# Optimization experiments

Measured on AMD Instinct MI355X. Metric: run time of the kernel, lower is better.

The kernel has to match this reference:

```python
import jax, jax.numpy as jnp
import numpy as np

EMB = 128
B, N = 8, 4096

def setup_inputs() -> dict:
    key = jax.random.key(0)
    k_x, k_q, k_k, k_v = jax.random.split(key, 4)
    return {
        "x": jax.random.normal(k_x, (B, N, EMB), dtype=jnp.float32),
        "w_query": jax.random.uniform(k_q, (EMB, EMB), dtype=jnp.float32),
        "w_key": jax.random.uniform(k_k, (EMB, EMB), dtype=jnp.float32),
        "w_value": jax.random.uniform(k_v, (EMB, EMB), dtype=jnp.float32),
    }

def reference(x, w_query, w_key, w_value):
    # QKV projections: [B, N, D]
    q = jnp.einsum("bnd,de->bne", x, w_query)
    k = jnp.einsum("bnd,de->bne", x, w_key)
    v = jnp.einsum("bnd,de->bne", x, w_value)
    dk = k.shape[-1]
    # scaled dot-product scores: [B, N, N]
    scale = jnp.einsum("bqd,bkd->bqk", q, k) / jnp.sqrt(jnp.float32(dk))
    probs = jax.nn.softmax(scale, axis=2)
    # attention output: [B, N, D]
    return jnp.einsum("bqk,bkd->bqd", probs, v)
```

## Files before the change

kernel.cpp:

```cpp
#include <hip/hip_runtime.h>
#include <hip/hip_bf16.h>

typedef __attribute__((ext_vector_type(4))) float  f32x4;
typedef __attribute__((ext_vector_type(8))) _Float16 h16x8;
typedef __attribute__((ext_vector_type(2))) __fp16 fp16x2;
typedef const __attribute__((address_space(1))) unsigned int guint;
typedef __attribute__((address_space(3))) unsigned int luint;

#define EMB 128
#define NSEQ 4096
#define NB 8
#define SCALE 0.08838834764831845f
#define QSC   (0.08838834764831845f * 1.44269504f)
#define NT    (NSEQ / 64)

#if __has_builtin(__builtin_amdgcn_exp2f)
#define EXP2(x) __builtin_amdgcn_exp2f(x)
#else
#define EXP2(x) exp2f(x)
#endif

__global__ void prep_w(const float* __restrict__ wq, const float* __restrict__ wk,
                       const float* __restrict__ wv, _Float16* __restrict__ whiT,
                       _Float16* __restrict__ wloT) {
    int idx = blockIdx.x * 256 + threadIdx.x;
    if (idx >= 3 * EMB * EMB) return;
    int widx = idx >> 14;
    int rem  = idx & 16383;
    int d = rem >> 7;
    int e = rem & 127;
    const float* w = (widx == 0) ? wq : (widx == 1) ? wk : wv;
    float v = w[d * 128 + e];
    _Float16 hi = (_Float16)v;
    _Float16 lo = (_Float16)(v - (float)hi);
    whiT[(size_t)widx * 16384 + (size_t)e * 128 + d] = hi;
    wloT[(size_t)widx * 16384 + (size_t)e * 128 + d] = lo;
}

__global__ __launch_bounds__(256) void qkv_proj(const float* __restrict__ x,
                                                const _Float16* __restrict__ whiT,
                                                const _Float16* __restrict__ wloT,
                                                _Float16* __restrict__ q,
                                                char* __restrict__ kimg,
                                                char* __restrict__ vimg,
                                                float* __restrict__ aq,
                                                float* __restrict__ ck) {
    const int widx = blockIdx.x >> 9;
    const int blk  = blockIdx.x & 511;
    const int lane = threadIdx.x & 63;
    const int wave = threadIdx.x >> 6;
    const int g    = lane >> 4;
    const int lr   = lane & 15;
    const int rb   = blk * 64 + wave * 16;

    h16x8 xhi[4], xlo[4];
    {
        const float* xrow = x + (size_t)(rb + lr) * EMB;
        #pragma unroll
        for (int kc = 0; kc < 4; ++kc) {
            const float* p = xrow + kc * 32 + g * 8;
            h16x8 ah, al;
            #pragma unroll
            for (int j = 0; j < 8; ++j) {
                float v = p[j];
                _Float16 h = (_Float16)v;
                ah[j] = h;
                al[j] = (_Float16)(v - (float)h);
            }
            xhi[kc] = ah;
            if (widx < 2) xlo[kc] = al;
        }
    }

    const int b  = rb >> 12;
    const int n0 = rb & 4095;

    f32x4 acc[8];
    #pragma unroll
    for (int ct = 0; ct < 8; ++ct) acc[ct] = (f32x4){0.f, 0.f, 0.f, 0.f};

    const _Float16* wh = whiT + (size_t)widx * 16384;
    const _Float16* wl = wloT + (size_t)widx * 16384;
    #pragma unroll
    for (int kc = 0; kc < 4; ++kc) {
        #pragma unroll
        for (int ct = 0; ct < 8; ++ct) {
            size_t off = (size_t)(ct * 16 + lr) * 128 + kc * 32 + g * 8;
            h16x8 bh = *(const h16x8*)(wh + off);
            acc[ct] = __builtin_amdgcn_mfma_f32_16x16x32_f16(xhi[kc], bh, acc[ct], 0, 0, 0);
            if (widx < 2) {
                h16x8 bl = *(const h16x8*)(wl + off);
                acc[ct] = __builtin_amdgcn_mfma_f32_16x16x32_f16(xlo[kc], bh, acc[ct], 0, 0, 0);
                acc[ct] = __builtin_amdgcn_mfma_f32_16x16x32_f16(xhi[kc], bl, acc[ct], 0, 0, 0);
            }
        }
    }

    if (widx < 2) {
        float c[4];
        #pragma unroll
        for (int r = 0; r < 4; ++r) {
            float rs = 0.f;
            #pragma unroll
            for (int ct = 0; ct < 8; ++ct) rs += acc[ct][r];
            #pragma unroll
            for (int off = 8; off; off >>= 1) rs += __shfl_xor(rs, off);
            c[r] = rs * (1.0f / 128.0f);
        }
        if (widx == 0) {
            #pragma unroll
            for (int ct = 0; ct < 8; ++ct)
                #pragma unroll
                for (int r = 0; r < 4; ++r) {
                    size_t row = rb + g * 4 + r;
                    q[row * 128 + ct * 16 + lr] = (_Float16)((acc[ct][r] - c[r]) * QSC);
                }
            if (lr == 0) {
                #pragma unroll
                for (int r = 0; r < 4; ++r) aq[rb + g * 4 + r] = c[r] * 128.0f * QSC;
            }
        } else {
            #pragma unroll
            for (int ct = 0; ct < 8; ++ct)
                #pragma unroll
                for (int r = 0; r < 4; ++r) {
                    int nn  = n0 + g * 4 + r;
                    int tt  = nn >> 6, r64 = nn & 63;
                    int slot = ((r64 >> 5) * 2 + ((r64 >> 2) & 1)) * 16
                             + (((r64 >> 3) & 3) << 2) + (r64 & 3);
                    int e = ct * 16 + lr;
                    size_t byte = ((size_t)(b * 64 + tt) << 14) + slot * 256
                                + ((2 * e) ^ ((slot & 15) << 4));
                    *(_Float16*)(kimg + byte) = (_Float16)(acc[ct][r] - c[r]);
                }
            if (lr == 0) {
                #pragma unroll
                for (int r = 0; r < 4; ++r) ck[rb + g * 4 + r] = c[r];
            }
        }
    } else {
        #pragma unroll
        for (int ct = 0; ct < 8; ++ct)
            #pragma unroll
            for (int r = 0; r < 4; ++r) {
                int e  = ct * 16 + lr;
                int nn = n0 + g * 4 + r;
                int tt = nn >> 6, kv = nn & 63;
                size_t byte = ((size_t)(b * 64 + tt) << 14) + e * 128
                            + ((2 * kv) ^ ((e & 7) << 4));
                *(_Float16*)(vimg + byte) = (_Float16)acc[ct][r];
            }
    }
}

__global__ __launch_bounds__(256, 2) void flash(const _Float16* __restrict__ q,
                                                const char* __restrict__ kimg,
                                                const char* __restrict__ vimg,
                                                const float* __restrict__ aq,
                                                const float* __restrict__ ck,
                                                float* __restrict__ O0,
                                                float* __restrict__ O1,
                                                float* __restrict__ m0a, float* __restrict__ l0a,
                                                float* __restrict__ m1a, float* __restrict__ l1a) {
    __shared__ __align__(16) char KsB[2][16384];
    __shared__ __align__(16) char VsB[2][16384];

    const int bp  = blockIdx.x;
    const int bid = (bp & 7) * 64 + (bp >> 3);

    const int lane = threadIdx.x & 63;
    const int wave = threadIdx.x >> 6;
    const int g    = lane >> 4;
    const int lr   = lane & 15;
    const int b    = bid >> 6;
    const int rem  = bid & 63;
    const int qt   = rem & 31;
    const int half = rem >> 5;
    const int t0   = half * (NT / 2);
    const size_t baseA = (size_t)b * NSEQ + qt * 128 + wave * 32;
    const size_t baseB = baseA + 16;

    float* __restrict__ Opart = half ? O1 : O0;
    float* __restrict__ mArr  = half ? m1a : m0a;
    float* __restrict__ lArr  = half ? l1a : l0a;

    const char* kimg_b = kimg + ((size_t)b << 20);
    const char* vimg_b = vimg + ((size_t)b << 20);
    const float* ckb   = ck + (size_t)b * NSEQ;

    h16x8 qfA[4], qfB[4];
    #pragma unroll
    for (int kc = 0; kc < 4; ++kc) {
        qfA[kc] = *(const h16x8*)(q + (baseA + lr) * 128 + kc * 32 + g * 8);
        qfB[kc] = *(const h16x8*)(q + (baseB + lr) * 128 + kc * 32 + g * 8);
    }
    const float aqvA = aq[baseA + lr];
    const float aqvB = aq[baseB + lr];

    auto stage = [&](int tile, int buf) {
        const char* ks = kimg_b + ((size_t)tile << 14) + wave * 4096 + lane * 16;
        const char* vs = vimg_b + ((size_t)tile << 14) + wave * 4096 + lane * 16;
        char* kd = (char*)KsB[buf] + wave * 4096;
        char* vd = (char*)VsB[buf] + wave * 4096;
        #pragma unroll
        for (int i = 0; i < 4; ++i) {
            __builtin_amdgcn_global_load_lds((guint*)(ks + i * 1024), (luint*)(kd + i * 1024), 16, 0, 0);
            __builtin_amdgcn_global_load_lds((guint*)(vs + i * 1024), (luint*)(vd + i * 1024), 16, 0, 0);
        }
    };

    stage(t0, 0);
    __syncthreads();

    f32x4 oA[8], oB[8];
    #pragma unroll
    for (int ct = 0; ct < 8; ++ct) {
        oA[ct] = (f32x4){0.f, 0.f, 0.f, 0.f};
        oB[ct] = (f32x4){0.f, 0.f, 0.f, 0.f};
    }
    float mA = -1e30f, mB = -1e30f;
    float lA = 0.f, lB = 0.f;

    int cur = 0;
    for (int t = t0; t < t0 + NT / 2; ++t) {
        int tn = (t + 1 < t0 + NT / 2) ? t + 1 : t;
        stage(tn, cur ^ 1);

        f32x4 ckt[4];
        #pragma unroll
        for (int ct = 0; ct < 4; ++ct)
            ckt[ct] = *(const f32x4*)(ckb + t * 64 + (ct >> 1) * 32 + (ct & 1) * 4 + g * 8);

        const char* Kb = KsB[cur];
        f32x4 sA[4], sB[4];
        __builtin_amdgcn_s_setprio(1);
        #pragma unroll
        for (int ct = 0; ct < 4; ++ct) {
            f32x4 aA = (f32x4){0.f, 0.f, 0.f, 0.f};
            f32x4 aB = (f32x4){0.f, 0.f, 0.f, 0.f};
            #pragma unroll
            for (int kc = 0; kc < 4; ++kc) {
                h16x8 kb = *(const h16x8*)(Kb + (ct * 16 + lr) * 256 + ((kc * 64 + g * 16) ^ (lr << 4)));
                aA = __builtin_amdgcn_mfma_f32_16x16x32_f16(kb, qfA[kc], aA, 0, 0, 0);
                aB = __builtin_amdgcn_mfma_f32_16x16x32_f16(kb, qfB[kc], aB, 0, 0, 0);
            }
            #pragma unroll
            for (int r = 0; r < 4; ++r) {
                aA[r] += aqvA * ckt[ct][r];
                aB[r] += aqvB * ckt[ct][r];
            }
            sA[ct] = aA;
            sB[ct] = aB;
        }
        __builtin_amdgcn_s_setprio(0);

        float tmA = sA[0][0], tmB = sB[0][0];
        #pragma unroll
        for (int ct = 0; ct < 4; ++ct)
            #pragma unroll
            for (int r = 0; r < 4; ++r) {
                tmA = fmaxf(tmA, sA[ct][r]);
                tmB = fmaxf(tmB, sB[ct][r]);
            }
        tmA = fmaxf(tmA, __shfl_xor(tmA, 16));
        tmA = fmaxf(tmA, __shfl_xor(tmA, 32));
        tmB = fmaxf(tmB, __shfl_xor(tmB, 16));
        tmB = fmaxf(tmB, __shfl_xor(tmB, 32));
        if (__any((tmA > mA + 11.544f) || (tmB > mB + 11.544f))) {
            float mnA = fmaxf(mA, tmA), mnB = fmaxf(mB, tmB);
            float scA = EXP2(mA - mnA), scB = EXP2(mB - mnB);
            mA = mnA; mB = mnB;
            lA *= scA; lB *= scB;
            float osA[4], osB[4];
            #pragma unroll
            for (int r = 0; r < 4; ++r) {
                osA[r] = __shfl(scA, (lane & 48) | (g * 4 + r));
                osB[r] = __shfl(scB, (lane & 48) | (g * 4 + r));
            }
            #pragma unroll
            for (int ct = 0; ct < 8; ++ct)
                #pragma unroll
                for (int r = 0; r < 4; ++r) {
                    oA[ct][r] *= osA[r];
                    oB[ct][r] *= osB[r];
                }
        }
        #pragma unroll
        for (int ct = 0; ct < 4; ++ct)
            #pragma unroll
            for (int r = 0; r < 4; ++r) {
                float pA = EXP2(sA[ct][r] - mA);
                float pB = EXP2(sB[ct][r] - mB);
                sA[ct][r] = pA; sB[ct][r] = pB;
                lA += pA; lB += pB;
            }

        union Pk { fp16x2 h2[4]; h16x8 v8; };
        h16x8 paA[2], paB[2];
        #pragma unroll
        for (int w = 0; w < 2; ++w) {
            Pk a, bk;
            a.h2[0]  = __builtin_amdgcn_cvt_pkrtz(sA[2 * w][0], sA[2 * w][1]);
            a.h2[1]  = __builtin_amdgcn_cvt_pkrtz(sA[2 * w][2], sA[2 * w][3]);
            a.h2[2]  = __builtin_amdgcn_cvt_pkrtz(sA[2 * w + 1][0], sA[2 * w + 1][1]);
            a.h2[3]  = __builtin_amdgcn_cvt_pkrtz(sA[2 * w + 1][2], sA[2 * w + 1][3]);
            bk.h2[0] = __builtin_amdgcn_cvt_pkrtz(sB[2 * w][0], sB[2 * w][1]);
            bk.h2[1] = __builtin_amdgcn_cvt_pkrtz(sB[2 * w][2], sB[2 * w][3]);
            bk.h2[2] = __builtin_amdgcn_cvt_pkrtz(sB[2 * w + 1][0], sB[2 * w + 1][1]);
            bk.h2[3] = __builtin_amdgcn_cvt_pkrtz(sB[2 * w + 1][2], sB[2 * w + 1][3]);
            paA[w] = a.v8;
            paB[w] = bk.v8;
        }

        const char* Vb = VsB[cur];
        __builtin_amdgcn_s_setprio(1);
        #pragma unroll
        for (int ct = 0; ct < 8; ++ct) {
            #pragma unroll
            for (int w = 0; w < 2; ++w) {
                h16x8 vb = *(const h16x8*)(Vb + (ct * 16 + lr) * 128 + ((w * 64 + g * 16) ^ ((lr & 7) << 4)));
                oA[ct] = __builtin_amdgcn_mfma_f32_16x16x32_f16(paA[w], vb, oA[ct], 0, 0, 0);
                oB[ct] = __builtin_amdgcn_mfma_f32_16x16x32_f16(paB[w], vb, oB[ct], 0, 0, 0);
            }
        }
        __builtin_amdgcn_s_setprio(0);

        __syncthreads();
        cur ^= 1;
    }

    lA += __shfl_xor(lA, 16);
    lA += __shfl_xor(lA, 32);
    lB += __shfl_xor(lB, 16);
    lB += __shfl_xor(lB, 32);
    if (lane < 16) {
        mArr[baseA + lr] = mA;  lArr[baseA + lr] = lA;
        mArr[baseB + lr] = mB;  lArr[baseB + lr] = lB;
    }
    #pragma unroll
    for (int ct = 0; ct < 8; ++ct)
        #pragma unroll
        for (int r = 0; r < 4; ++r) {
            size_t rowA = baseA + g * 4 + r;
            size_t rowB = baseB + g * 4 + r;
            Opart[rowA * EMB + ct * 16 + lr] = oA[ct][r];
            Opart[rowB * EMB + ct * 16 + lr] = oB[ct][r];
        }
}

__global__ __launch_bounds__(256) void merge_halves(const float* __restrict__ O1,
                                                    const float* __restrict__ m0a,
                                                    const float* __restrict__ l0a,
                                                    const float* __restrict__ m1a,
                                                    const float* __restrict__ l1a,
                                                    float* __restrict__ out) {
    int gid = blockIdx.x * 256 + threadIdx.x;
    int row = gid >> 4;
    int c0  = (gid & 15) * 8;
    float mm0 = m0a[row], mm1 = m1a[row];
    float M   = fmaxf(mm0, mm1);
    float w0  = EXP2(mm0 - M), w1 = EXP2(mm1 - M);
    float inv = 1.0f / (l0a[row] * w0 + l1a[row] * w1);
    float*       p0 = out + (size_t)row * EMB + c0;
    const float* p1 = O1  + (size_t)row * EMB + c0;
    f32x4 a0 = *(const f32x4*)p0, a1 = *(const f32x4*)(p0 + 4);
    f32x4 b0 = *(const f32x4*)p1, b1 = *(const f32x4*)(p1 + 4);
    f32x4 r0 = (a0 * w0 + b0 * w1) * inv;
    f32x4 r1 = (a1 * w0 + b1 * w1) * inv;
    *(f32x4*)p0       = r0;
    *(f32x4*)(p0 + 4) = r1;
}

extern "C" void kernel_launch(void* const* d_in, const int* in_sizes, int n_in,
                              void* d_out, int out_size, void* d_ws, size_t ws_size,
                              hipStream_t stream) {
    const float* x  = (const float*)d_in[0];
    const float* wq = (const float*)d_in[1];
    const float* wk = (const float*)d_in[2];
    const float* wv = (const float*)d_in[3];

    char* ws = (char*)d_ws;
    _Float16* q    = (_Float16*)(ws);
    char*     kimg = (char*)    (ws + 8388608);
    char*     vimg = (char*)    (ws + 16777216);
    float*    aq   = (float*)   (ws + 25165824);
    float*    ck   = (float*)   (ws + 25296896);
    _Float16* whiT = (_Float16*)(ws + 25427968);
    _Float16* wloT = (_Float16*)(ws + 25526272);
    float*    O1   = (float*)   (ws + 25690112);
    float*    m0a  = (float*)   (ws + 42467328);
    float*    l0a  = (float*)   (ws + 42598400);
    float*    m1a  = (float*)   (ws + 42729472);
    float*    l1a  = (float*)   (ws + 42860544);

    prep_w<<<192, 256, 0, stream>>>(wq, wk, wv, whiT, wloT);
    qkv_proj<<<1536, 256, 0, stream>>>(x, whiT, wloT, q, kimg, vimg, aq, ck);
    flash<<<512, 256, 0, stream>>>(q, kimg, vimg, aq, ck,
                                   (float*)d_out, O1, m0a, l0a, m1a, l1a);
    merge_halves<<<2048, 256, 0, stream>>>(O1, m0a, l0a, m1a, l1a, (float*)d_out);
}
```

Measured before the change: 143.7 us.

## Shrink KV tiles to 32, raise occupancy, and split KV four ways

Cuts the K/V tile from 64 to 32 keys, rewriting the K and V image layouts and swizzles so shared memory per block halves, and raises launch bounds to 4 blocks per SM. When the workspace is large enough, the key range is split into 4 chunks instead of 2, launching more blocks, and a generalized n-way merge kernel combines the partials. This aims to raise occupancy and parallelism so latency is better hidden. In exchange it adds more partial-output traffic, a heavier merge, and more loop iterations with synchronization per tile.

New measurement: 310.7 us. +116.3%, slower.

```diff
diff --git a/kernel.cpp b/kernel.cpp
--- a/kernel.cpp
+++ b/kernel.cpp
@@ -12,7 +12,7 @@
 #define NB 8
 #define SCALE 0.08838834764831845f
 #define QSC   (0.08838834764831845f * 1.44269504f)
-#define NT    (NSEQ / 64)
+#define NTT   (NSEQ / 32)
 
 #if __has_builtin(__builtin_amdgcn_exp2f)
 #define EXP2(x) __builtin_amdgcn_exp2f(x)
@@ -124,12 +124,11 @@
             for (int ct = 0; ct < 8; ++ct)
                 #pragma unroll
                 for (int r = 0; r < 4; ++r) {
-                    int nn  = n0 + g * 4 + r;
-                    int tt  = nn >> 6, r64 = nn & 63;
-                    int slot = ((r64 >> 5) * 2 + ((r64 >> 2) & 1)) * 16
-                             + (((r64 >> 3) & 3) << 2) + (r64 & 3);
-                    int e = ct * 16 + lr;
-                    size_t byte = ((size_t)(b * 64 + tt) << 14) + slot * 256
+                    int nn   = n0 + g * 4 + r;
+                    int tt   = nn >> 5, r32 = nn & 31;
+                    int slot = ((r32 >> 2) & 1) * 16 + (r32 >> 3) * 4 + (r32 & 3);
+                    int e    = ct * 16 + lr;
+                    size_t byte = ((size_t)(b * 128 + tt) << 13) + slot * 256
                                 + ((2 * e) ^ ((slot & 15) << 4));
                     *(_Float16*)(kimg + byte) = (_Float16)(acc[ct][r] - c[r]);
                 }
@@ -145,44 +144,46 @@
             for (int r = 0; r < 4; ++r) {
                 int e  = ct * 16 + lr;
                 int nn = n0 + g * 4 + r;
-                int tt = nn >> 6, kv = nn & 63;
-                size_t byte = ((size_t)(b * 64 + tt) << 14) + e * 128
-                            + ((2 * kv) ^ ((e & 7) << 4));
+                int tt = nn >> 5, kv = nn & 31;
+                size_t byte = ((size_t)(b * 128 + tt) << 13) + e * 64
+                            + ((2 * kv) ^ (((e >> 1) & 3) << 4));
                 *(_Float16*)(vimg + byte) = (_Float16)acc[ct][r];
             }
     }
 }
 
-__global__ __launch_bounds__(256, 2) void flash(const _Float16* __restrict__ q,
+__global__ __launch_bounds__(256, 4) void flash(const _Float16* __restrict__ q,
                                                 const char* __restrict__ kimg,
                                                 const char* __restrict__ vimg,
                                                 const float* __restrict__ aq,
                                                 const float* __restrict__ ck,
                                                 float* __restrict__ O0,
-                                                float* __restrict__ O1,
-                                                float* __restrict__ m0a, float* __restrict__ l0a,
-                                                float* __restrict__ m1a, float* __restrict__ l1a) {
-    __shared__ __align__(16) char KsB[2][16384];
-    __shared__ __align__(16) char VsB[2][16384];
-
-    const int bp  = blockIdx.x;
-    const int bid = (bp & 7) * 64 + (bp >> 3);
+                                                float* __restrict__ Oext,
+                                                float* __restrict__ mArr,
+                                                float* __restrict__ lArr,
+                                                int nsplit, int cnt) {
+    __shared__ __align__(16) char KsB[2][8192];
+    __shared__ __align__(16) char VsB[2][8192];
+
+    const int nblk = 256 * nsplit;
+    const int bp   = blockIdx.x;
+    const int bid  = (bp & 7) * (nblk >> 3) + (bp >> 3);
 
     const int lane = threadIdx.x & 63;
     const int wave = threadIdx.x >> 6;
     const int g    = lane >> 4;
     const int lr   = lane & 15;
-    const int b    = bid >> 6;
-    const int rem  = bid & 63;
-    const int qt   = rem & 31;
-    const int half = rem >> 5;
-    const int t0   = half * (NT / 2);
+    const int sp   = bid % nsplit;
+    const int rest = bid / nsplit;
+    const int qt   = rest & 31;
+    const int b    = rest >> 5;
+    const int t0   = sp * cnt;
     const size_t baseA = (size_t)b * NSEQ + qt * 128 + wave * 32;
     const size_t baseB = baseA + 16;
 
-    float* __restrict__ Opart = half ? O1 : O0;
-    float* __restrict__ mArr  = half ? m1a : m0a;
-    float* __restrict__ lArr  = half ? l1a : l0a;
+    float* __restrict__ Opart = (sp == 0) ? O0 : Oext + (size_t)(sp - 1) * NB * NSEQ * EMB;
+    float* __restrict__ mOut  = mArr + (size_t)sp * (NB * NSEQ);
+    float* __restrict__ lOut  = lArr + (size_t)sp * (NB * NSEQ);
 
     const char* kimg_b = kimg + ((size_t)b << 20);
     const char* vimg_b = vimg + ((size_t)b << 20);
@@ -198,12 +199,12 @@
     const float aqvB = aq[baseB + lr];
 
     auto stage = [&](int tile, int buf) {
-        const char* ks = kimg_b + ((size_t)tile << 14) + wave * 4096 + lane * 16;
-        const char* vs = vimg_b + ((size_t)tile << 14) + wave * 4096 + lane * 16;
-        char* kd = (char*)KsB[buf] + wave * 4096;
-        char* vd = (char*)VsB[buf] + wave * 4096;
-        #pragma unroll
-        for (int i = 0; i < 4; ++i) {
+        const char* ks = kimg_b + ((size_t)tile << 13) + wave * 2048 + lane * 16;
+        const char* vs = vimg_b + ((size_t)tile << 13) + wave * 2048 + lane * 16;
+        char* kd = (char*)KsB[buf] + wave * 2048;
+        char* vd = (char*)VsB[buf] + wave * 2048;
+        #pragma unroll
+        for (int i = 0; i < 2; ++i) {
             __builtin_amdgcn_global_load_lds((guint*)(ks + i * 1024), (luint*)(kd + i * 1024), 16, 0, 0);
             __builtin_amdgcn_global_load_lds((guint*)(vs + i * 1024), (luint*)(vd + i * 1024), 16, 0, 0);
         }
@@ -222,20 +223,18 @@
     float lA = 0.f, lB = 0.f;
 
     int cur = 0;
-    for (int t = t0; t < t0 + NT / 2; ++t) {
-        int tn = (t + 1 < t0 + NT / 2) ? t + 1 : t;
+    for (int t = t0; t < t0 + cnt; ++t) {
+        int tn = (t + 1 < t0 + cnt) ? t + 1 : t;
         stage(tn, cur ^ 1);
 
-        f32x4 ckt[4];
-        #pragma unroll
-        for (int ct = 0; ct < 4; ++ct)
-            ckt[ct] = *(const f32x4*)(ckb + t * 64 + (ct >> 1) * 32 + (ct & 1) * 4 + g * 8);
+        f32x4 ckt0 = *(const f32x4*)(ckb + t * 32 + g * 8);
+        f32x4 ckt1 = *(const f32x4*)(ckb + t * 32 + g * 8 + 4);
 
         const char* Kb = KsB[cur];
-        f32x4 sA[4], sB[4];
+        f32x4 sA[2], sB[2];
         __builtin_amdgcn_s_setprio(1);
         #pragma unroll
-        for (int ct = 0; ct < 4; ++ct) {
+        for (int ct = 0; ct < 2; ++ct) {
             f32x4 aA = (f32x4){0.f, 0.f, 0.f, 0.f};
             f32x4 aB = (f32x4){0.f, 0.f, 0.f, 0.f};
             #pragma unroll
@@ -244,10 +243,11 @@
                 aA = __builtin_amdgcn_mfma_f32_16x16x32_f16(kb, qfA[kc], aA, 0, 0, 0);
                 aB = __builtin_amdgcn_mfma_f32_16x16x32_f16(kb, qfB[kc], aB, 0, 0, 0);
             }
+            f32x4 ckt = ct ? ckt1 : ckt0;
             #pragma unroll
             for (int r = 0; r < 4; ++r) {
-                aA[r] += aqvA * ckt[ct][r];
-                aB[r] += aqvB * ckt[ct][r];
+                aA[r] += aqvA * ckt[r];
+                aB[r] += aqvB * ckt[r];
             }
             sA[ct] = aA;
             sB[ct] = aB;
@@ -256,7 +256,7 @@
 
         float tmA = sA[0][0], tmB = sB[0][0];
         #pragma unroll
-        for (int ct = 0; ct < 4; ++ct)
+        for (int ct = 0; ct < 2; ++ct)
             #pragma unroll
             for (int r = 0; r < 4; ++r) {
                 tmA = fmaxf(tmA, sA[ct][r]);
@@ -286,7 +286,7 @@
                 }
         }
         #pragma unroll
-        for (int ct = 0; ct < 4; ++ct)
+        for (int ct = 0; ct < 2; ++ct)
             #pragma unroll
             for (int r = 0; r < 4; ++r) {
                 float pA = EXP2(sA[ct][r] - mA);
@@ -296,32 +296,24 @@
             }
 
         union Pk { fp16x2 h2[4]; h16x8 v8; };
-        h16x8 paA[2], paB[2];
-        #pragma unroll
-        for (int w = 0; w < 2; ++w) {
-            Pk a, bk;
-            a.h2[0]  = __builtin_amdgcn_cvt_pkrtz(sA[2 * w][0], sA[2 * w][1]);
-            a.h2[1]  = __builtin_amdgcn_cvt_pkrtz(sA[2 * w][2], sA[2 * w][3]);
-            a.h2[2]  = __builtin_amdgcn_cvt_pkrtz(sA[2 * w + 1][0], sA[2 * w + 1][1]);
-            a.h2[3]  = __builtin_amdgcn_cvt_pkrtz(sA[2 * w + 1][2], sA[2 * w + 1][3]);
-            bk.h2[0] = __builtin_amdgcn_cvt_pkrtz(sB[2 * w][0], sB[2 * w][1]);
-            bk.h2[1] = __builtin_amdgcn_cvt_pkrtz(sB[2 * w][2], sB[2 * w][3]);
-            bk.h2[2] = __builtin_amdgcn_cvt_pkrtz(sB[2 * w + 1][0], sB[2 * w + 1][1]);
-            bk.h2[3] = __builtin_amdgcn_cvt_pkrtz(sB[2 * w + 1][2], sB[2 * w + 1][3]);
-            paA[w] = a.v8;
-            paB[w] = bk.v8;
-        }
+        Pk pkA, pkB;
+        pkA.h2[0] = __builtin_amdgcn_cvt_pkrtz(sA[0][0], sA[0][1]);
+        pkA.h2[1] = __builtin_amdgcn_cvt_pkrtz(sA[0][2], sA[0][3]);
+        pkA.h2[2] = __builtin_amdgcn_cvt_pkrtz(sA[1][0], sA[1][1]);
+        pkA.h2[3] = __builtin_amdgcn_cvt_pkrtz(sA[1][2], sA[1][3]);
+        pkB.h2[0] = __builtin_amdgcn_cvt_pkrtz(sB[0][0], sB[0][1]);
+        pkB.h2[1] = __builtin_amdgcn_cvt_pkrtz(sB[0][2], sB[0][3]);
+        pkB.h2[2] = __builtin_amdgcn_cvt_pkrtz(sB[1][0], sB[1][1]);
+        pkB.h2[3] = __builtin_amdgcn_cvt_pkrtz(sB[1][2], sB[1][3]);
+        h16x8 paA = pkA.v8, paB = pkB.v8;
 
         const char* Vb = VsB[cur];
         __builtin_amdgcn_s_setprio(1);
         #pragma unroll
         for (int ct = 0; ct < 8; ++ct) {
-            #pragma unroll
-            for (int w = 0; w < 2; ++w) {
-                h16x8 vb = *(const h16x8*)(Vb + (ct * 16 + lr) * 128 + ((w * 64 + g * 16) ^ ((lr & 7) << 4)));
-                oA[ct] = __builtin_amdgcn_mfma_f32_16x16x32_f16(paA[w], vb, oA[ct], 0, 0, 0);
-                oB[ct] = __builtin_amdgcn_mfma_f32_16x16x32_f16(paB[w], vb, oB[ct], 0, 0, 0);
-            }
+            h16x8 vb = *(const h16x8*)(Vb + (ct * 16 + lr) * 64 + ((g * 16) ^ (((lr >> 1) & 3) << 4)));
+            oA[ct] = __builtin_amdgcn_mfma_f32_16x16x32_f16(paA, vb, oA[ct], 0, 0, 0);
+            oB[ct] = __builtin_amdgcn_mfma_f32_16x16x32_f16(paB, vb, oB[ct], 0, 0, 0);
         }
         __builtin_amdgcn_s_setprio(0);
 
@@ -334,8 +326,8 @@
     lB += __shfl_xor(lB, 16);
     lB += __shfl_xor(lB, 32);
     if (lane < 16) {
-        mArr[baseA + lr] = mA;  lArr[baseA + lr] = lA;
-        mArr[baseB + lr] = mB;  lArr[baseB + lr] = lB;
+        mOut[baseA + lr] = mA;  lOut[baseA + lr] = lA;
+        mOut[baseB + lr] = mB;  lOut[baseB + lr] = lB;
     }
     #pragma unroll
     for (int ct = 0; ct < 8; ++ct)
@@ -348,27 +340,30 @@
         }
 }
 
-__global__ __launch_bounds__(256) void merge_halves(const float* __restrict__ O1,
-                                                    const float* __restrict__ m0a,
-                                                    const float* __restrict__ l0a,
-                                                    const float* __restrict__ m1a,
-                                                    const float* __restrict__ l1a,
-                                                    float* __restrict__ out) {
+__global__ __launch_bounds__(256) void merge_n(const float* __restrict__ Oext,
+                                               const float* __restrict__ mArr,
+                                               const float* __restrict__ lArr,
+                                               float* __restrict__ out, int nsplit) {
     int gid = blockIdx.x * 256 + threadIdx.x;
     int row = gid >> 4;
     int c0  = (gid & 15) * 8;
-    float mm0 = m0a[row], mm1 = m1a[row];
-    float M   = fmaxf(mm0, mm1);
-    float w0  = EXP2(mm0 - M), w1 = EXP2(mm1 - M);
-    float inv = 1.0f / (l0a[row] * w0 + l1a[row] * w1);
-    float*       p0 = out + (size_t)row * EMB + c0;
-    const float* p1 = O1  + (size_t)row * EMB + c0;
-    f32x4 a0 = *(const f32x4*)p0, a1 = *(const f32x4*)(p0 + 4);
-    f32x4 b0 = *(const f32x4*)p1, b1 = *(const f32x4*)(p1 + 4);
-    f32x4 r0 = (a0 * w0 + b0 * w1) * inv;
-    f32x4 r1 = (a1 * w0 + b1 * w1) * inv;
-    *(f32x4*)p0       = r0;
-    *(f32x4*)(p0 + 4) = r1;
+    float M = mArr[row];
+    for (int p = 1; p < nsplit; ++p) M = fmaxf(M, mArr[p * (NB * NSEQ) + row]);
+    f32x4 a0 = (f32x4){0.f, 0.f, 0.f, 0.f}, a1 = a0;
+    float wsum = 0.f;
+    for (int p = 0; p < nsplit; ++p) {
+        float wp = EXP2(mArr[p * (NB * NSEQ) + row] - M);
+        wsum += lArr[p * (NB * NSEQ) + row] * wp;
+        const float* src = (p == 0) ? (out + (size_t)row * EMB + c0)
+                                    : (Oext + (size_t)(p - 1) * NB * NSEQ * EMB
+                                       + (size_t)row * EMB + c0);
+        a0 += *(const f32x4*)src * wp;
+        a1 += *(const f32x4*)(src + 4) * wp;
+    }
+    float inv = 1.0f / wsum;
+    float* p0 = out + (size_t)row * EMB + c0;
+    *(f32x4*)p0       = a0 * inv;
+    *(f32x4*)(p0 + 4) = a1 * inv;
 }
 
 extern "C" void kernel_launch(void* const* d_in, const int* in_sizes, int n_in,
@@ -387,15 +382,22 @@
     float*    ck   = (float*)   (ws + 25296896);
     _Float16* whiT = (_Float16*)(ws + 25427968);
     _Float16* wloT = (_Float16*)(ws + 25526272);
-    float*    O1   = (float*)   (ws + 25690112);
-    float*    m0a  = (float*)   (ws + 42467328);
-    float*    l0a  = (float*)   (ws + 42598400);
-    float*    m1a  = (float*)   (ws + 42729472);
-    float*    l1a  = (float*)   (ws + 42860544);
+
+    const size_t PART = 25690112;
+    const size_t OSZ  = (size_t)NB * NSEQ * EMB * 4;
+    const size_t MLSZ = (size_t)NB * NSEQ * 4;
+
+    size_t need4 = PART + 3 * OSZ + 8 * MLSZ;
+    int nsplit = (ws_size >= need4) ? 4 : 2;
+    int cnt = NTT / nsplit;
+
+    float* Oext = (float*)(ws + PART);
+    float* mArr = (float*)(ws + PART + (size_t)(nsplit - 1) * OSZ);
+    float* lArr = mArr + (size_t)nsplit * (NB * NSEQ);
 
     prep_w<<<192, 256, 0, stream>>>(wq, wk, wv, whiT, wloT);
     qkv_proj<<<1536, 256, 0, stream>>>(x, whiT, wloT, q, kimg, vimg, aq, ck);
-    flash<<<512, 256, 0, stream>>>(q, kimg, vimg, aq, ck,
-                                   (float*)d_out, O1, m0a, l0a, m1a, l1a);
-    merge_halves<<<2048, 256, 0, stream>>>(O1, m0a, l0a, m1a, l1a, (float*)d_out);
+    flash<<<256 * nsplit, 256, 0, stream>>>(q, kimg, vimg, aq, ck,
+                                            (float*)d_out, Oext, mArr, lArr, nsplit, cnt);
+    merge_n<<<2048, 256, 0, stream>>>(Oext, mArr, lArr, (float*)d_out, nsplit);
 }
```
